# Performance work log

Measured on AMD Instinct MI355X. Metric: run time of the kernel, lower is better.

The kernel has to match this reference:

```python
import jax, jax.numpy as jnp
import numpy as np

B, T, C = 4, 2048, 1024
H = 16
DH = C // H
DFF = 4 * C


def _layernorm(x, g, b, eps=1e-5):
    mu = jnp.mean(x, axis=-1, keepdims=True)
    var = jnp.var(x, axis=-1, keepdims=True)
    return (x - mu) * jax.lax.rsqrt(var + eps) * g + b


def setup_inputs() -> dict:
    key = jax.random.key(0)
    ks = jax.random.split(key, 12)
    s = 0.02
    return {
        "x": jax.random.normal(ks[0], (B, T, C), jnp.float32),
        "Wq": jax.random.normal(ks[1], (H, C, DH), jnp.float32) * s,
        "bq": jnp.zeros((H, DH), jnp.float32),
        "Wk": jax.random.normal(ks[2], (H, C, DH), jnp.float32) * s,
        "bk": jnp.zeros((H, DH), jnp.float32),
        "Wv": jax.random.normal(ks[3], (H, C, DH), jnp.float32) * s,
        "bv": jnp.zeros((H, DH), jnp.float32),
        "Wo": jax.random.normal(ks[4], (C, C), jnp.float32) * s,
        "bo": jnp.zeros((C,), jnp.float32),
        "ln1_g": jnp.ones((C,), jnp.float32),
        "ln1_b": jnp.zeros((C,), jnp.float32),
        "ln2_g": jnp.ones((C,), jnp.float32),
        "ln2_b": jnp.zeros((C,), jnp.float32),
        "W1": jax.random.normal(ks[5], (C, DFF), jnp.float32) * s,
        "b1": jnp.zeros((DFF,), jnp.float32),
        "W2": jax.random.normal(ks[6], (DFF, C), jnp.float32) * s,
        "b2": jnp.zeros((C,), jnp.float32),
    }


def reference(x, Wq, bq, Wk, bk, Wv, bv, Wo, bo, ln1_g, ln1_b, ln2_g, ln2_b, W1, b1, W2, b2):
    # pre-norm for attention
    xn = _layernorm(x, ln1_g, ln1_b)
    # per-head projections, batched: [B,H,T,DH]
    q = jnp.einsum("btc,hcd->bhtd", xn, Wq) + bq[None, :, None, :]
    k = jnp.einsum("btc,hcd->bhtd", xn, Wk) + bk[None, :, None, :]
    v = jnp.einsum("btc,hcd->bhtd", xn, Wv) + bv[None, :, None, :]
    # FAITHFUL to source: scores / scale with scale = DH**-0.5, i.e. * sqrt(DH)
    scores = jnp.einsum("bhtd,bhsd->bhts", q, k) * jnp.sqrt(jnp.float32(DH))
    attn = jax.nn.softmax(scores, axis=-1)
    o = jnp.einsum("bhts,bhsd->bhtd", attn, v)  # [B,H,T,DH]
    # concat heads along last dim (head order matches ModuleList concat)
    o = jnp.transpose(o, (0, 2, 1, 3)).reshape(B, T, C)
    attn_out = o @ Wo + bo  # dropout is identity at eval
    x = x + attn_out
    xn2 = _layernorm(x, ln2_g, ln2_b)
    ffn = jax.nn.relu(xn2 @ W1 + b1) @ W2 + b2
    return x + ffn
```

## Files before the change

kernel.cpp:

```cpp
#include <hip/hip_runtime.h>
#include <hip/hip_bf16.h>
#include <stdint.h>

typedef unsigned short ushort_t;
typedef short short8 __attribute__((ext_vector_type(8)));
typedef unsigned short ushortx8 __attribute__((ext_vector_type(8)));
typedef float floatx4 __attribute__((ext_vector_type(4)));

__device__ __forceinline__ float b2f(ushort_t u) {
    return __uint_as_float(((unsigned int)u) << 16);
}
__device__ __forceinline__ ushort_t f2bf(float f) {
    unsigned int u = __float_as_uint(f);
    unsigned int r = u + 0x7FFFu + ((u >> 16) & 1u);
    return (ushort_t)(r >> 16);
}
__device__ __forceinline__ unsigned int cvtpk(float lo, float hi) {
    unsigned int r;
    asm("v_cvt_pk_bf16_f32 %0, %1, %2" : "=v"(r) : "v"(lo), "v"(hi));
    return r;
}
__device__ __forceinline__ void gll16(const void* g, void* l) {
    __builtin_amdgcn_global_load_lds((const __attribute__((address_space(1))) unsigned int*)g,
                                     (__attribute__((address_space(3))) unsigned int*)l,
                                     16, 0, 0);
}

__global__ void transpose_kernel(const float* __restrict__ in, ushort_t* __restrict__ out,
                                 int K, int N) {
    __shared__ float tile[32][33];
    in += (long)blockIdx.z * K * N;
    out += (long)blockIdx.z * K * N;
    int k0 = blockIdx.x * 32, n0 = blockIdx.y * 32;
    int x = threadIdx.x, y = threadIdx.y;
#pragma unroll
    for (int i = 0; i < 4; i++)
        tile[y + 8 * i][x] = in[(long)(k0 + y + 8 * i) * N + n0 + x];
    __syncthreads();
#pragma unroll
    for (int i = 0; i < 4; i++)
        out[(long)(n0 + y + 8 * i) * K + k0 + x] = f2bf(tile[x][y + 8 * i]);
}

__global__ void concat_bias_kernel(const float* __restrict__ bq, const float* __restrict__ bk,
                                   const float* __restrict__ bv, float* __restrict__ dst) {
    int i = blockIdx.x * 256 + threadIdx.x;
    dst[i] = i < 1024 ? bq[i] : (i < 2048 ? bk[i - 1024] : bv[i - 2048]);
}

__global__ __launch_bounds__(256) void ln_kernel(const float* __restrict__ in,
                                                 ushort_t* __restrict__ out,
                                                 const float* __restrict__ g,
                                                 const float* __restrict__ b) {
    long row = blockIdx.x;
    int tid = threadIdx.x;
    float4 v4 = *((const float4*)(in + row * 1024) + tid);
    float v[4] = {v4.x, v4.y, v4.z, v4.w};
    float s1 = v[0] + v[1] + v[2] + v[3];
    float s2 = v[0] * v[0] + v[1] * v[1] + v[2] * v[2] + v[3] * v[3];
#pragma unroll
    for (int m = 32; m >= 1; m >>= 1) {
        s1 += __shfl_xor(s1, m);
        s2 += __shfl_xor(s2, m);
    }
    __shared__ float r1[4], r2[4];
    int w = tid >> 6;
    if ((tid & 63) == 0) { r1[w] = s1; r2[w] = s2; }
    __syncthreads();
    s1 = r1[0] + r1[1] + r1[2] + r1[3];
    s2 = r2[0] + r2[1] + r2[2] + r2[3];
    float mu = s1 * (1.0f / 1024.0f);
    float var = s2 * (1.0f / 1024.0f) - mu * mu;
    float inv = rsqrtf(var + 1e-5f);
    float y[4];
#pragma unroll
    for (int i = 0; i < 4; i++)
        y[i] = (v[i] - mu) * inv * g[tid * 4 + i] + b[tid * 4 + i];
    unsigned int lo = (unsigned int)f2bf(y[0]) | ((unsigned int)f2bf(y[1]) << 16);
    unsigned int hi = (unsigned int)f2bf(y[2]) | ((unsigned int)f2bf(y[3]) << 16);
    *(uint2*)(out + row * 1024 + tid * 4) = make_uint2(lo, hi);
}

template <typename OutT, int RELU, int MODE>
__device__ __forceinline__ void gemm128(
    const ushort_t* __restrict__ A, int lda,
    const ushort_t* __restrict__ Bt, int ldb, int K,
    OutT* __restrict__ C, long cBatch, int ldc,
    const float* __restrict__ bias, const float* __restrict__ resid,
    ushort_t* As, ushort_t* Bs) {
    int m0 = blockIdx.x * 128, n0 = blockIdx.y * 128;
    int tid = threadIdx.x, lane = tid & 63, w = tid >> 6;
    int ln = lane & 15, quad = lane >> 4;
    int wr = w >> 1, wc = w & 1;
    int lr = lane >> 2, lc = (lane & 3) * 8;

    auto stage = [&](int k0, int buf) {
#pragma unroll
        for (int i = 0; i < 4; i++) {
            int id = w * 4 + i;
            int blk = id & 7;
            int row = blk * 16 + lr;
            if (id < 8)
                gll16(A + (long)(m0 + row) * lda + k0 + lc, As + buf * 4096 + blk * 512);
            else
                gll16(Bt + (long)(n0 + row) * ldb + k0 + lc, Bs + buf * 4096 + blk * 512);
        }
    };

    floatx4 acc[4][4];
#pragma unroll
    for (int a = 0; a < 4; a++)
#pragma unroll
        for (int bb = 0; bb < 4; bb++) acc[a][bb] = floatx4{0, 0, 0, 0};

    stage(0, 0);
    int cur = 0;
    for (int k0 = 0; k0 < K; k0 += 32, cur ^= 1) {
        __syncthreads();
        if (k0 + 32 < K) stage(k0 + 32, cur ^ 1);
        const ushort_t* Ab = As + cur * 4096;
        const ushort_t* Bb = Bs + cur * 4096;
        short8 af[4], bf[4];
#pragma unroll
        for (int j = 0; j < 4; j++) {
            af[j] = *(const short8*)(Ab + (wr * 64 + j * 16 + ln) * 32 + quad * 8);
            bf[j] = *(const short8*)(Bb + (wc * 64 + j * 16 + ln) * 32 + quad * 8);
        }
#pragma unroll
        for (int a = 0; a < 4; a++)
#pragma unroll
            for (int bb = 0; bb < 4; bb++)
                acc[a][bb] = __builtin_amdgcn_mfma_f32_16x16x32_bf16(af[a], bf[bb], acc[a][bb], 0, 0, 0);
    }
#pragma unroll
    for (int bb = 0; bb < 4; bb++) {
        int gn = n0 + wc * 64 + bb * 16 + ln;
        float bv = bias ? bias[gn] : 0.0f;
#pragma unroll
        for (int a = 0; a < 4; a++) {
#pragma unroll
            for (int r = 0; r < 4; r++) {
                int gm = m0 + wr * 64 + a * 16 + quad * 4 + r;
                float val = acc[a][bb][r] + bv;
                if (RELU) val = fmaxf(val, 0.0f);
                if constexpr (MODE == 2) {
                    int gnl = gn & 1023;
                    long off;
                    if (gn < 2048)
                        off = (long)(gn >> 10) * 8388608 + (long)(gm >> 11) * 2097152 +
                              (long)(gm & 2047) * 1024 + gnl;
                    else
                        off = 16777216L +
                              ((((long)(gm >> 11)) * 16 + (gnl >> 6)) * 64 + (gnl & 63)) * 2048 +
                              (gm & 2047);
                    C[off] = (OutT)f2bf(val);
                } else {
                    long off = (long)(gm >> 11) * cBatch + (long)(gm & 2047) * ldc + gn;
                    if (resid) val += resid[off];
                    if constexpr (sizeof(OutT) == 2)
                        C[off] = (OutT)f2bf(val);
                    else
                        C[off] = (OutT)val;
                }
            }
        }
    }
}

__global__ __launch_bounds__(256) void gemm128_qkv_kernel(
    const ushort_t* __restrict__ A, const ushort_t* __restrict__ Bt,
    ushort_t* __restrict__ C, const float* __restrict__ bias) {
    __shared__ ushort_t As[2 * 128 * 32];
    __shared__ ushort_t Bs[2 * 128 * 32];
    gemm128<ushort_t, 0, 2>(A, 1024, Bt, 1024, 1024, C, 0, 0, bias, nullptr, As, Bs);
}

__global__ __launch_bounds__(256) void gemm128_bf16_relu_kernel(
    const ushort_t* __restrict__ A, int lda, const ushort_t* __restrict__ Bt, int ldb, int K,
    ushort_t* __restrict__ C, long cBatch, int ldc, const float* __restrict__ bias) {
    __shared__ ushort_t As[2 * 128 * 32];
    __shared__ ushort_t Bs[2 * 128 * 32];
    gemm128<ushort_t, 1, 0>(A, lda, Bt, ldb, K, C, cBatch, ldc, bias, nullptr, As, Bs);
}

__global__ __launch_bounds__(256) void gemm128_f32_kernel(
    const ushort_t* __restrict__ A, int lda, const ushort_t* __restrict__ Bt, int ldb, int K,
    float* __restrict__ C, long cBatch, int ldc,
    const float* __restrict__ bias, const float* __restrict__ resid) {
    __shared__ ushort_t As[2 * 128 * 32];
    __shared__ ushort_t Bs[2 * 128 * 32];
    gemm128<float, 0, 0>(A, lda, Bt, ldb, K, C, cBatch, ldc, bias, resid, As, Bs);
}

__global__ __launch_bounds__(512, 4) void attn_kernel(
    const ushort_t* __restrict__ q, const ushort_t* __restrict__ k,
    const ushort_t* __restrict__ vt, ushort_t* __restrict__ o) {
    __shared__ ushort_t Klds[2 * 4096];
    __shared__ ushort_t Vlds[2 * 4096];
    int flat = blockIdx.x;
    int bh = (flat & 7) * 8 + (flat >> 6);
    int xt = (flat >> 3) & 7;
    int b = bh >> 4, h = bh & 15;
    int t0 = xt * 256;
    int tid = threadIdx.x, lane = tid & 63, w = tid >> 6;
    int ln = lane & 15, quad = lane >> 4;
    int lr = lane >> 2, lq = lane & 3;
    int bsrc = (lane & 48) + ((lane >> 4) << 2);
    int rsw = (ln >> 1) & 3;
    int ssw = (lr >> 1) & 3;

    const ushort_t* qbase = q + ((long)b * 2048 + t0 + w * 32) * 1024 + h * 64;
    short8 qf[2][2];
#pragma unroll
    for (int sub = 0; sub < 2; sub++)
#pragma unroll
        for (int s = 0; s < 2; s++) {
            ushortx8 t = *(const ushortx8*)(qbase + (long)(sub * 16 + ln) * 1024 + s * 32 + quad * 8);
#pragma unroll
            for (int j = 0; j < 8; j++) qf[sub][s][j] = (short)f2bf(b2f(t[j]) * 8.0f);
        }

    floatx4 O[2][4];
    float m_i[2] = {-1e30f, -1e30f}, l_i[2] = {0.0f, 0.0f};
#pragma unroll
    for (int sub = 0; sub < 2; sub++)
#pragma unroll
        for (int i = 0; i < 4; i++) O[sub][i] = floatx4{0, 0, 0, 0};

    long krow0 = (long)b * 2048 * 1024 + h * 64;
    const ushort_t* vbase = vt + (long)bh * 64 * 2048;

    auto stage = [&](int kv0, int buf) {
#pragma unroll
        for (int i = 0; i < 2; i++) {
            int id = w * 2 + i;
            int s = (id >> 2) & 1, qt = id & 3;
            int cs = ((lq ^ ssw) << 3);
            if (id < 8) {
                int prow = ((qt >> 1) << 5) + ((lr >> 2) << 3) + ((qt & 1) << 2) + (lr & 3);
                gll16(k + krow0 + (long)(kv0 + prow) * 1024 + s * 32 + cs,
                      Klds + buf * 4096 + s * 2048 + qt * 512);
            } else {
                int row = qt * 16 + lr;
                gll16(vbase + (long)row * 2048 + kv0 + s * 32 + cs,
                      Vlds + buf * 4096 + s * 2048 + qt * 512);
            }
        }
    };

    stage(0, 0);
    int cur = 0;
    for (int t32 = 0; t32 < 32; t32++, cur ^= 1) {
        __syncthreads();
        if (t32 < 31) stage((t32 + 1) * 64, cur ^ 1);
        const ushort_t* Kb = Klds + cur * 4096;
        const ushort_t* Vb = Vlds + cur * 4096;

        floatx4 Z[2][4];
#pragma unroll
        for (int sub = 0; sub < 2; sub++)
#pragma unroll
            for (int nc = 0; nc < 4; nc++) Z[sub][nc] = floatx4{0, 0, 0, 0};
#pragma unroll
        for (int s = 0; s < 2; s++)
#pragma unroll
            for (int nc = 0; nc < 4; nc++) {
                short8 kf = *(const short8*)(Kb + s * 2048 + (nc * 16 + ln) * 32 + ((quad ^ rsw) << 3));
                Z[0][nc] = __builtin_amdgcn_mfma_f32_16x16x32_bf16(kf, qf[0][s], Z[0][nc], 0, 0, 0);
                Z[1][nc] = __builtin_amdgcn_mfma_f32_16x16x32_bf16(kf, qf[1][s], Z[1][nc], 0, 0, 0);
            }

        float alpha[2];
        short8 pf[2][2];
#pragma unroll
        for (int sub = 0; sub < 2; sub++) {
            float mx = -1e30f;
#pragma unroll
            for (int nc = 0; nc < 4; nc++)
#pragma unroll
                for (int r = 0; r < 4; r++) mx = fmaxf(mx, Z[sub][nc][r]);
            mx = fmaxf(mx, __shfl_xor(mx, 16));
            mx = fmaxf(mx, __shfl_xor(mx, 32));
            float nm = fmaxf(m_i[sub], mx);
            alpha[sub] = __expf(m_i[sub] - nm);
            m_i[sub] = nm;
            float rs = 0.0f;
#pragma unroll
            for (int s = 0; s < 2; s++) {
                float a0 = __expf(Z[sub][2 * s][0] - nm), a1 = __expf(Z[sub][2 * s][1] - nm);
                float a2 = __expf(Z[sub][2 * s][2] - nm), a3 = __expf(Z[sub][2 * s][3] - nm);
                float b0 = __expf(Z[sub][2 * s + 1][0] - nm), b1 = __expf(Z[sub][2 * s + 1][1] - nm);
                float b2 = __expf(Z[sub][2 * s + 1][2] - nm), b3 = __expf(Z[sub][2 * s + 1][3] - nm);
                rs += ((a0 + a1) + (a2 + a3)) + ((b0 + b1) + (b2 + b3));
                union { unsigned int u[4]; short8 v; } pu;
                pu.u[0] = cvtpk(a0, a1);
                pu.u[1] = cvtpk(a2, a3);
                pu.u[2] = cvtpk(b0, b1);
                pu.u[3] = cvtpk(b2, b3);
                pf[sub][s] = pu.v;
            }
            rs += __shfl_xor(rs, 16);
            rs += __shfl_xor(rs, 32);
            l_i[sub] = l_i[sub] * alpha[sub] + rs;
        }
#pragma unroll
        for (int sub = 0; sub < 2; sub++)
#pragma unroll
            for (int r = 0; r < 4; r++) {
                float ar = __shfl(alpha[sub], bsrc + r);
#pragma unroll
                for (int dc = 0; dc < 4; dc++) O[sub][dc][r] *= ar;
            }
#pragma unroll
        for (int s = 0; s < 2; s++)
#pragma unroll
            for (int dc = 0; dc < 4; dc++) {
                short8 vf = *(const short8*)(Vb + s * 2048 + (dc * 16 + ln) * 32 + ((quad ^ rsw) << 3));
                O[0][dc] = __builtin_amdgcn_mfma_f32_16x16x32_bf16(pf[0][s], vf, O[0][dc], 0, 0, 0);
                O[1][dc] = __builtin_amdgcn_mfma_f32_16x16x32_bf16(pf[1][s], vf, O[1][dc], 0, 0, 0);
            }
    }
#pragma unroll
    for (int sub = 0; sub < 2; sub++)
#pragma unroll
        for (int r = 0; r < 4; r++) {
            float inv = 1.0f / __shfl(l_i[sub], bsrc + r);
            int t = t0 + w * 32 + sub * 16 + quad * 4 + r;
            ushort_t* orow = o + ((long)b * 2048 + t) * 1024 + h * 64;
#pragma unroll
            for (int dc = 0; dc < 4; dc++) orow[dc * 16 + ln] = f2bf(O[sub][dc][r] * inv);
        }
}

extern "C" void kernel_launch(void* const* d_in, const int* in_sizes, int n_in,
                              void* d_out, int out_size, void* d_ws, size_t ws_size,
                              hipStream_t stream) {
    const float* x   = (const float*)d_in[0];
    const float* Wq  = (const float*)d_in[1];
    const float* bq  = (const float*)d_in[2];
    const float* Wk  = (const float*)d_in[3];
    const float* bk  = (const float*)d_in[4];
    const float* Wv  = (const float*)d_in[5];
    const float* bv  = (const float*)d_in[6];
    const float* Wo  = (const float*)d_in[7];
    const float* bo  = (const float*)d_in[8];
    const float* g1  = (const float*)d_in[9];
    const float* be1 = (const float*)d_in[10];
    const float* g2  = (const float*)d_in[11];
    const float* be2 = (const float*)d_in[12];
    const float* W1  = (const float*)d_in[13];
    const float* b1  = (const float*)d_in[14];
    const float* W2  = (const float*)d_in[15];
    const float* b2  = (const float*)d_in[16];
    float* out = (float*)d_out;

    const long MB = 1 << 20;
    char* w = (char*)d_ws;
    ushort_t* xn  = (ushort_t*)(w);
    float*    x2  = (float*)(w + 16 * MB);
    ushort_t* qb  = (ushort_t*)(w + 48 * MB);
    ushort_t* kb  = (ushort_t*)(w + 64 * MB);
    ushort_t* vtb = (ushort_t*)(w + 80 * MB);
    ushort_t* xn2 = qb;
    ushort_t* h1  = (ushort_t*)(w + 64 * MB);
    ushort_t* WqT = (ushort_t*)(w + 96 * MB);
    ushort_t* WkT = (ushort_t*)(w + 98 * MB);
    ushort_t* WvT = (ushort_t*)(w + 100 * MB);
    ushort_t* WoT = (ushort_t*)(w + 102 * MB);
    ushort_t* W1T = (ushort_t*)(w + 104 * MB);
    ushort_t* W2T = (ushort_t*)(w + 112 * MB);
    float* biasCat = x2;

    dim3 tb(32, 8);
    transpose_kernel<<<dim3(32, 2, 16), tb, 0, stream>>>(Wq, WqT, 1024, 64);
    transpose_kernel<<<dim3(32, 2, 16), tb, 0, stream>>>(Wk, WkT, 1024, 64);
    transpose_kernel<<<dim3(32, 2, 16), tb, 0, stream>>>(Wv, WvT, 1024, 64);
    transpose_kernel<<<dim3(32, 32, 1), tb, 0, stream>>>(Wo, WoT, 1024, 1024);
    transpose_kernel<<<dim3(32, 128, 1), tb, 0, stream>>>(W1, W1T, 1024, 4096);
    transpose_kernel<<<dim3(128, 32, 1), tb, 0, stream>>>(W2, W2T, 4096, 1024);
    concat_bias_kernel<<<12, 256, 0, stream>>>(bq, bk, bv, biasCat);

    ln_kernel<<<8192, 256, 0, stream>>>(x, xn, g1, be1);
    gemm128_qkv_kernel<<<dim3(64, 24), 256, 0, stream>>>(xn, WqT, qb, biasCat);
    attn_kernel<<<512, 512, 0, stream>>>(qb, kb, vtb, xn );
    gemm128_f32_kernel<<<dim3(64, 8), 256, 0, stream>>>(xn, 1024, WoT, 1024, 1024,
                                                        x2, 2048L * 1024, 1024, bo, x);
    ln_kernel<<<8192, 256, 0, stream>>>((const float*)x2, xn2, g2, be2);
    gemm128_bf16_relu_kernel<<<dim3(64, 16), 256, 0, stream>>>(
        xn2, 1024, W1T, 1024, 1024, h1, 2048L * 2048, 2048, b1);
    gemm128_f32_kernel<<<dim3(64, 8), 256, 0, stream>>>(
        h1, 2048, W2T, 4096, 2048, out, 2048L * 1024, 1024, b2, x2);
    gemm128_bf16_relu_kernel<<<dim3(64, 16), 256, 0, stream>>>(
        xn2, 1024, W1T + 2048L * 1024, 1024, 1024, h1, 2048L * 2048, 2048, b1 + 2048);
    gemm128_f32_kernel<<<dim3(64, 8), 256, 0, stream>>>(
        h1, 2048, W2T + 2048, 4096, 2048, out, 2048L * 1024, 1024, nullptr, out);
}
```

Before: 594.2 us.

## Add 256x256 GEMM with 4-stage LDS pipeline for QKV and FFN-up

Introduces a new gemm256 kernel with 512 threads and 256x256 output tiles. It uses a four-buffer global_load_lds pipeline with manual vmcnt waits, barriers and setprio around the MFMA phases, plus an XCD-aware block remap. The QKV projection and both W1 ReLU GEMMs now use it, while the Wo and W2 GEMMs stay on the 128-tile kernel. Larger tiles raise data reuse per load and the deeper pipeline hides memory latency, at the cost of more registers and LDS. The fixed grids of 384 and 256 blocks can underfill the CUs.

```diff
diff --git a/kernel.cpp b/kernel.cpp
--- a/kernel.cpp
+++ b/kernel.cpp
@@ -6,6 +6,9 @@
 typedef short short8 __attribute__((ext_vector_type(8)));
 typedef unsigned short ushortx8 __attribute__((ext_vector_type(8)));
 typedef float floatx4 __attribute__((ext_vector_type(4)));
+
+template <int N> struct IC { static constexpr int value = N; };
+template <bool B> struct BC { static constexpr bool value = B; };
 
 __device__ __forceinline__ float b2f(ushort_t u) {
     return __uint_as_float(((unsigned int)u) << 16);
@@ -143,9 +146,138 @@
                 int gm = m0 + wr * 64 + a * 16 + quad * 4 + r;
                 float val = acc[a][bb][r] + bv;
                 if (RELU) val = fmaxf(val, 0.0f);
+                long off = (long)(gm >> 11) * cBatch + (long)(gm & 2047) * ldc + gn;
+                if (resid) val += resid[off];
+                if constexpr (sizeof(OutT) == 2)
+                    C[off] = (OutT)f2bf(val);
+                else
+                    C[off] = (OutT)val;
+            }
+        }
+    }
+}
+
+__global__ __launch_bounds__(256) void gemm128_f32_kernel(
+    const ushort_t* __restrict__ A, int lda, const ushort_t* __restrict__ Bt, int ldb, int K,
+    float* __restrict__ C, long cBatch, int ldc,
+    const float* __restrict__ bias, const float* __restrict__ resid) {
+    __shared__ ushort_t As[2 * 128 * 32];
+    __shared__ ushort_t Bs[2 * 128 * 32];
+    gemm128<float, 0, 0>(A, lda, Bt, ldb, K, C, cBatch, ldc, bias, resid, As, Bs);
+}
+
+template <int RELU, int MODE>
+__device__ __forceinline__ void gemm256(
+    const ushort_t* __restrict__ A, int lda,
+    const ushort_t* __restrict__ Bt, int ldb, int K, int ntn,
+    ushort_t* __restrict__ C, long cBatch, int ldc,
+    const float* __restrict__ bias, ushort_t* lds) {
+    int nwg = gridDim.x;
+    int wg = ((int)blockIdx.x & 7) * (nwg >> 3) + ((int)blockIdx.x >> 3);
+    int m0 = (wg / ntn) * 256, n0 = (wg % ntn) * 256;
+    int tid = threadIdx.x, lane = tid & 63, w = tid >> 6;
+    int ln = lane & 15, quad = lane >> 4;
+    int wm = w >> 2, wn = w & 3;
+    int lr = lane >> 2, lq = lane & 3;
+    int ssw = (lr >> 1) & 3, rsw = (ln >> 1) & 3;
+
+    const ushort_t* pa[2];
+    const ushort_t* pb[2];
+#pragma unroll
+    for (int i = 0; i < 2; i++) {
+        int id = w * 2 + i;
+        pa[i] = A + (long)(m0 + id * 16 + lr) * lda + ((lq ^ ssw) << 3);
+        pb[i] = Bt + (long)(n0 + id * 16 + lr) * ldb + ((lq ^ ssw) << 3);
+    }
+    auto stageA = [&](int t) {
+        ushort_t* d = lds + (t & 3) * 16384;
+#pragma unroll
+        for (int i = 0; i < 2; i++) gll16(pa[i] + t * 32, d + (w * 2 + i) * 512);
+    };
+    auto stageB = [&](int t) {
+        ushort_t* d = lds + (t & 3) * 16384 + 8192;
+#pragma unroll
+        for (int i = 0; i < 2; i++) gll16(pb[i] + t * 32, d + (w * 2 + i) * 512);
+    };
+
+    floatx4 acc[8][4];
+#pragma unroll
+    for (int a = 0; a < 8; a++)
+#pragma unroll
+        for (int bb = 0; bb < 4; bb++) acc[a][bb] = floatx4{0, 0, 0, 0};
+
+    stageA(0); stageB(0); stageA(1); stageB(1); stageA(2); stageB(2);
+    asm volatile("s_waitcnt vmcnt(8)" ::: "memory");
+    __builtin_amdgcn_s_barrier();
+    __builtin_amdgcn_sched_barrier(0);
+
+    int NT = K >> 5;
+    auto iter = [&](int t, auto vmc, auto stc) {
+        constexpr int VM = decltype(vmc)::value;
+        constexpr bool ST = decltype(stc)::value;
+        const ushort_t* Ab = lds + (t & 3) * 16384;
+        const ushort_t* Bb = Ab + 8192;
+        short8 af[4], bf[4];
+#pragma unroll
+        for (int j = 0; j < 4; j++)
+            bf[j] = *(const short8*)(Bb + (wn * 64 + j * 16 + ln) * 32 + ((quad ^ rsw) << 3));
+#pragma unroll
+        for (int j = 0; j < 4; j++)
+            af[j] = *(const short8*)(Ab + (wm * 128 + j * 16 + ln) * 32 + ((quad ^ rsw) << 3));
+        if constexpr (ST) stageA(t + 3);
+        __builtin_amdgcn_s_barrier();
+        __builtin_amdgcn_sched_barrier(0);
+        __builtin_amdgcn_s_setprio(1);
+#pragma unroll
+        for (int a = 0; a < 4; a++)
+#pragma unroll
+            for (int bb = 0; bb < 4; bb++)
+                acc[a][bb] = __builtin_amdgcn_mfma_f32_16x16x32_bf16(af[a], bf[bb], acc[a][bb], 0, 0, 0);
+        __builtin_amdgcn_s_setprio(0);
+        __builtin_amdgcn_s_barrier();
+        __builtin_amdgcn_sched_barrier(0);
+#pragma unroll
+        for (int j = 0; j < 4; j++)
+            af[j] = *(const short8*)(Ab + (wm * 128 + 64 + j * 16 + ln) * 32 + ((quad ^ rsw) << 3));
+        if constexpr (ST) stageB(t + 3);
+        __builtin_amdgcn_s_barrier();
+        __builtin_amdgcn_sched_barrier(0);
+        __builtin_amdgcn_s_setprio(1);
+#pragma unroll
+        for (int a = 0; a < 4; a++)
+#pragma unroll
+            for (int bb = 0; bb < 4; bb++)
+                acc[a + 4][bb] = __builtin_amdgcn_mfma_f32_16x16x32_bf16(af[a], bf[bb], acc[a + 4][bb], 0, 0, 0);
+        __builtin_amdgcn_s_setprio(0);
+        if constexpr (VM == 8)
+            asm volatile("s_waitcnt vmcnt(8)" ::: "memory");
+        else if constexpr (VM == 4)
+            asm volatile("s_waitcnt vmcnt(4)" ::: "memory");
+        else
+            asm volatile("s_waitcnt vmcnt(0)" ::: "memory");
+        __builtin_amdgcn_s_barrier();
+        __builtin_amdgcn_sched_barrier(0);
+    };
+
+    for (int t = 0; t < NT - 3; ++t) iter(t, IC<8>{}, BC<true>{});
+    iter(NT - 3, IC<4>{}, BC<false>{});
+    iter(NT - 2, IC<0>{}, BC<false>{});
+    iter(NT - 1, IC<0>{}, BC<false>{});
+
+#pragma unroll
+    for (int bb = 0; bb < 4; bb++) {
+        int gn = n0 + wn * 64 + bb * 16 + ln;
+        float bv = bias[gn];
+#pragma unroll
+        for (int a = 0; a < 8; a++) {
+#pragma unroll
+            for (int r = 0; r < 4; r++) {
+                int gm = m0 + wm * 128 + a * 16 + quad * 4 + r;
+                float val = acc[a][bb][r] + bv;
+                if (RELU) val = fmaxf(val, 0.0f);
+                long off;
                 if constexpr (MODE == 2) {
                     int gnl = gn & 1023;
-                    long off;
                     if (gn < 2048)
                         off = (long)(gn >> 10) * 8388608 + (long)(gm >> 11) * 2097152 +
                               (long)(gm & 2047) * 1024 + gnl;
@@ -153,43 +285,27 @@
                         off = 16777216L +
                               ((((long)(gm >> 11)) * 16 + (gnl >> 6)) * 64 + (gnl & 63)) * 2048 +
                               (gm & 2047);
-                    C[off] = (OutT)f2bf(val);
                 } else {
-                    long off = (long)(gm >> 11) * cBatch + (long)(gm & 2047) * ldc + gn;
-                    if (resid) val += resid[off];
-                    if constexpr (sizeof(OutT) == 2)
-                        C[off] = (OutT)f2bf(val);
-                    else
-                        C[off] = (OutT)val;
+                    off = (long)(gm >> 11) * cBatch + (long)(gm & 2047) * ldc + gn;
                 }
+                C[off] = f2bf(val);
             }
         }
     }
 }
 
-__global__ __launch_bounds__(256) void gemm128_qkv_kernel(
+__global__ __launch_bounds__(512, 2) void gemm256_qkv_kernel(
     const ushort_t* __restrict__ A, const ushort_t* __restrict__ Bt,
     ushort_t* __restrict__ C, const float* __restrict__ bias) {
-    __shared__ ushort_t As[2 * 128 * 32];
-    __shared__ ushort_t Bs[2 * 128 * 32];
-    gemm128<ushort_t, 0, 2>(A, 1024, Bt, 1024, 1024, C, 0, 0, bias, nullptr, As, Bs);
-}
-
-__global__ __launch_bounds__(256) void gemm128_bf16_relu_kernel(
-    const ushort_t* __restrict__ A, int lda, const ushort_t* __restrict__ Bt, int ldb, int K,
-    ushort_t* __restrict__ C, long cBatch, int ldc, const float* __restrict__ bias) {
-    __shared__ ushort_t As[2 * 128 * 32];
-    __shared__ ushort_t Bs[2 * 128 * 32];
-    gemm128<ushort_t, 1, 0>(A, lda, Bt, ldb, K, C, cBatch, ldc, bias, nullptr, As, Bs);
-}
-
-__global__ __launch_bounds__(256) void gemm128_f32_kernel(
-    const ushort_t* __restrict__ A, int lda, const ushort_t* __restrict__ Bt, int ldb, int K,
-    float* __restrict__ C, long cBatch, int ldc,
-    const float* __restrict__ bias, const float* __restrict__ resid) {
-    __shared__ ushort_t As[2 * 128 * 32];
-    __shared__ ushort_t Bs[2 * 128 * 32];
-    gemm128<float, 0, 0>(A, lda, Bt, ldb, K, C, cBatch, ldc, bias, resid, As, Bs);
+    __shared__ ushort_t lds[4 * 16384];
+    gemm256<0, 2>(A, 1024, Bt, 1024, 1024, 12, C, 0, 0, bias, lds);
+}
+
+__global__ __launch_bounds__(512, 2) void gemm256_relu_kernel(
+    const ushort_t* __restrict__ A, const ushort_t* __restrict__ Bt,
+    ushort_t* __restrict__ C, const float* __restrict__ bias) {
+    __shared__ ushort_t lds[4 * 16384];
+    gemm256<1, 0>(A, 1024, Bt, 1024, 1024, 8, C, 2048L * 2048, 2048, bias, lds);
 }
 
 __global__ __launch_bounds__(512, 4) void attn_kernel(
@@ -381,17 +497,15 @@
     concat_bias_kernel<<<12, 256, 0, stream>>>(bq, bk, bv, biasCat);
 
     ln_kernel<<<8192, 256, 0, stream>>>(x, xn, g1, be1);
-    gemm128_qkv_kernel<<<dim3(64, 24), 256, 0, stream>>>(xn, WqT, qb, biasCat);
+    gemm256_qkv_kernel<<<384, 512, 0, stream>>>(xn, WqT, qb, biasCat);
     attn_kernel<<<512, 512, 0, stream>>>(qb, kb, vtb, xn );
     gemm128_f32_kernel<<<dim3(64, 8), 256, 0, stream>>>(xn, 1024, WoT, 1024, 1024,
                                                         x2, 2048L * 1024, 1024, bo, x);
     ln_kernel<<<8192, 256, 0, stream>>>((const float*)x2, xn2, g2, be2);
-    gemm128_bf16_relu_kernel<<<dim3(64, 16), 256, 0, stream>>>(
-        xn2, 1024, W1T, 1024, 1024, h1, 2048L * 2048, 2048, b1);
+    gemm256_relu_kernel<<<256, 512, 0, stream>>>(xn2, W1T, h1, b1);
     gemm128_f32_kernel<<<dim3(64, 8), 256, 0, stream>>>(
         h1, 2048, W2T, 4096, 2048, out, 2048L * 1024, 1024, b2, x2);
-    gemm128_bf16_relu_kernel<<<dim3(64, 16), 256, 0, stream>>>(
-        xn2, 1024, W1T + 2048L * 1024, 1024, 1024, h1, 2048L * 2048, 2048, b1 + 2048);
+    gemm256_relu_kernel<<<256, 512, 0, stream>>>(xn2, W1T + 2048L * 1024, h1, b1 + 2048);
     gemm128_f32_kernel<<<dim3(64, 8), 256, 0, stream>>>(
         h1, 2048, W2T + 2048, 4096, 2048, out, 2048L * 1024, 1024, nullptr, out);
 }
```

After: 592.6 us. About the same (-0.3%).

## Triple-buffer GEMM LDS with swizzled layout, raw barriers and XCD-aware tile mapping

Applied to the files above, without the earlier changes.

Changes the shared GEMM from double to triple buffering, keeping two global-to-LDS stages in flight with explicit vmcnt waits and raw s_barrier instead of __syncthreads. LDS columns are XOR-swizzled on write and read to avoid bank conflicts, and source pointers are precomputed once. Launches become 1D with an XCD-aware remap of block index to tile, so neighbouring tiles share L2 on the same chiplet. LDS use per block grows to 48KB, and the hand-placed waitcnt/barrier sequence must stay correct.

```diff
diff --git a/kernel.cpp b/kernel.cpp
--- a/kernel.cpp
+++ b/kernel.cpp
@@ -6,6 +6,8 @@
 typedef short short8 __attribute__((ext_vector_type(8)));
 typedef unsigned short ushortx8 __attribute__((ext_vector_type(8)));
 typedef float floatx4 __attribute__((ext_vector_type(4)));
+
+#define SBAR() asm volatile("s_barrier" ::: "memory")
 
 __device__ __forceinline__ float b2f(ushort_t u) {
     return __uint_as_float(((unsigned int)u) << 16);
@@ -87,24 +89,28 @@
     const ushort_t* __restrict__ Bt, int ldb, int K,
     OutT* __restrict__ C, long cBatch, int ldc,
     const float* __restrict__ bias, const float* __restrict__ resid,
-    ushort_t* As, ushort_t* Bs) {
-    int m0 = blockIdx.x * 128, n0 = blockIdx.y * 128;
+    ushort_t* As, ushort_t* Bs, int mT, int nT) {
+    int m0 = mT * 128, n0 = nT * 128;
     int tid = threadIdx.x, lane = tid & 63, w = tid >> 6;
     int ln = lane & 15, quad = lane >> 4;
     int wr = w >> 1, wc = w & 1;
-    int lr = lane >> 2, lc = (lane & 3) * 8;
-
-    auto stage = [&](int k0, int buf) {
-#pragma unroll
-        for (int i = 0; i < 4; i++) {
-            int id = w * 4 + i;
-            int blk = id & 7;
-            int row = blk * 16 + lr;
-            if (id < 8)
-                gll16(A + (long)(m0 + row) * lda + k0 + lc, As + buf * 4096 + blk * 512);
-            else
-                gll16(Bt + (long)(n0 + row) * ldb + k0 + lc, Bs + buf * 4096 + blk * 512);
-        }
+    int lr = lane >> 2, lq = lane & 3;
+    int ssw = (lr >> 1) & 3, rsw = (ln >> 1) & 3;
+
+    const ushort_t* src[4];
+    ushort_t* dstb[4];
+#pragma unroll
+    for (int i = 0; i < 4; i++) {
+        int id = w * 4 + i;
+        int blk = id & 7;
+        int row = blk * 16 + lr;
+        src[i] = (id < 8 ? A + (long)(m0 + row) * lda
+                         : Bt + (long)(n0 + row) * ldb) + ((lq ^ ssw) << 3);
+        dstb[i] = (id < 8 ? As : Bs) + blk * 512;
+    }
+    auto stage = [&](int t, int buf) {
+#pragma unroll
+        for (int i = 0; i < 4; i++) gll16(src[i] + t * 32, dstb[i] + buf * 4096);
     };
 
     floatx4 acc[4][4];
@@ -113,25 +119,40 @@
 #pragma unroll
         for (int bb = 0; bb < 4; bb++) acc[a][bb] = floatx4{0, 0, 0, 0};
 
+    int NT = K >> 5;
     stage(0, 0);
-    int cur = 0;
-    for (int k0 = 0; k0 < K; k0 += 32, cur ^= 1) {
-        __syncthreads();
-        if (k0 + 32 < K) stage(k0 + 32, cur ^ 1);
+    stage(1, 1);
+    asm volatile("s_waitcnt vmcnt(4)" ::: "memory");
+    SBAR();
+
+    int cur = 0, bst = 2;
+    auto body = [&](int t, int doStage, int vm) {
+        if (doStage) stage(t + 2, bst);
         const ushort_t* Ab = As + cur * 4096;
         const ushort_t* Bb = Bs + cur * 4096;
         short8 af[4], bf[4];
 #pragma unroll
         for (int j = 0; j < 4; j++) {
-            af[j] = *(const short8*)(Ab + (wr * 64 + j * 16 + ln) * 32 + quad * 8);
-            bf[j] = *(const short8*)(Bb + (wc * 64 + j * 16 + ln) * 32 + quad * 8);
+            af[j] = *(const short8*)(Ab + (wr * 64 + j * 16 + ln) * 32 + ((quad ^ rsw) << 3));
+            bf[j] = *(const short8*)(Bb + (wc * 64 + j * 16 + ln) * 32 + ((quad ^ rsw) << 3));
         }
 #pragma unroll
         for (int a = 0; a < 4; a++)
 #pragma unroll
             for (int bb = 0; bb < 4; bb++)
                 acc[a][bb] = __builtin_amdgcn_mfma_f32_16x16x32_bf16(af[a], bf[bb], acc[a][bb], 0, 0, 0);
-    }
+        if (vm == 4)
+            asm volatile("s_waitcnt vmcnt(4)" ::: "memory");
+        else if (vm == 0)
+            asm volatile("s_waitcnt vmcnt(0)" ::: "memory");
+        SBAR();
+        cur = cur == 2 ? 0 : cur + 1;
+        bst = bst == 2 ? 0 : bst + 1;
+    };
+    for (int t = 0; t < NT - 2; ++t) body(t, 1, 4);
+    body(NT - 2, 0, 0);
+    body(NT - 1, 0, -1);
+
 #pragma unroll
     for (int bb = 0; bb < 4; bb++) {
         int gn = n0 + wc * 64 + bb * 16 + ln;
@@ -167,29 +188,39 @@
     }
 }
 
-__global__ __launch_bounds__(256) void gemm128_qkv_kernel(
+__device__ __forceinline__ int xcd_swz(int flat, int nwg) {
+    return (flat & 7) * (nwg >> 3) + (flat >> 3);
+}
+
+__global__ __launch_bounds__(256, 3) void gemm128_qkv_kernel(
     const ushort_t* __restrict__ A, const ushort_t* __restrict__ Bt,
     ushort_t* __restrict__ C, const float* __restrict__ bias) {
-    __shared__ ushort_t As[2 * 128 * 32];
-    __shared__ ushort_t Bs[2 * 128 * 32];
-    gemm128<ushort_t, 0, 2>(A, 1024, Bt, 1024, 1024, C, 0, 0, bias, nullptr, As, Bs);
-}
-
-__global__ __launch_bounds__(256) void gemm128_bf16_relu_kernel(
+    __shared__ ushort_t As[3 * 4096];
+    __shared__ ushort_t Bs[3 * 4096];
+    int wg = xcd_swz(blockIdx.x, gridDim.x);
+    gemm128<ushort_t, 0, 2>(A, 1024, Bt, 1024, 1024, C, 0, 0, bias, nullptr,
+                            As, Bs, wg & 63, wg >> 6);
+}
+
+__global__ __launch_bounds__(256, 3) void gemm128_relu_kernel(
     const ushort_t* __restrict__ A, int lda, const ushort_t* __restrict__ Bt, int ldb, int K,
     ushort_t* __restrict__ C, long cBatch, int ldc, const float* __restrict__ bias) {
-    __shared__ ushort_t As[2 * 128 * 32];
-    __shared__ ushort_t Bs[2 * 128 * 32];
-    gemm128<ushort_t, 1, 0>(A, lda, Bt, ldb, K, C, cBatch, ldc, bias, nullptr, As, Bs);
-}
-
-__global__ __launch_bounds__(256) void gemm128_f32_kernel(
+    __shared__ ushort_t As[3 * 4096];
+    __shared__ ushort_t Bs[3 * 4096];
+    int wg = xcd_swz(blockIdx.x, gridDim.x);
+    gemm128<ushort_t, 1, 0>(A, lda, Bt, ldb, K, C, cBatch, ldc, bias, nullptr,
+                            As, Bs, wg & 63, wg >> 6);
+}
+
+__global__ __launch_bounds__(256, 3) void gemm128_f32_kernel(
     const ushort_t* __restrict__ A, int lda, const ushort_t* __restrict__ Bt, int ldb, int K,
     float* __restrict__ C, long cBatch, int ldc,
     const float* __restrict__ bias, const float* __restrict__ resid) {
-    __shared__ ushort_t As[2 * 128 * 32];
-    __shared__ ushort_t Bs[2 * 128 * 32];
-    gemm128<float, 0, 0>(A, lda, Bt, ldb, K, C, cBatch, ldc, bias, resid, As, Bs);
+    __shared__ ushort_t As[3 * 4096];
+    __shared__ ushort_t Bs[3 * 4096];
+    int wg = xcd_swz(blockIdx.x, gridDim.x);
+    gemm128<float, 0, 0>(A, lda, Bt, ldb, K, C, cBatch, ldc, bias, resid,
+                         As, Bs, wg & 63, wg >> 6);
 }
 
 __global__ __launch_bounds__(512, 4) void attn_kernel(
@@ -381,17 +412,17 @@
     concat_bias_kernel<<<12, 256, 0, stream>>>(bq, bk, bv, biasCat);
 
     ln_kernel<<<8192, 256, 0, stream>>>(x, xn, g1, be1);
-    gemm128_qkv_kernel<<<dim3(64, 24), 256, 0, stream>>>(xn, WqT, qb, biasCat);
+    gemm128_qkv_kernel<<<1536, 256, 0, stream>>>(xn, WqT, qb, biasCat);
     attn_kernel<<<512, 512, 0, stream>>>(qb, kb, vtb, xn );
-    gemm128_f32_kernel<<<dim3(64, 8), 256, 0, stream>>>(xn, 1024, WoT, 1024, 1024,
-                                                        x2, 2048L * 1024, 1024, bo, x);
+    gemm128_f32_kernel<<<512, 256, 0, stream>>>(xn, 1024, WoT, 1024, 1024,
+                                                x2, 2048L * 1024, 1024, bo, x);
     ln_kernel<<<8192, 256, 0, stream>>>((const float*)x2, xn2, g2, be2);
-    gemm128_bf16_relu_kernel<<<dim3(64, 16), 256, 0, stream>>>(
+    gemm128_relu_kernel<<<1024, 256, 0, stream>>>(
         xn2, 1024, W1T, 1024, 1024, h1, 2048L * 2048, 2048, b1);
-    gemm128_f32_kernel<<<dim3(64, 8), 256, 0, stream>>>(
+    gemm128_f32_kernel<<<512, 256, 0, stream>>>(
         h1, 2048, W2T, 4096, 2048, out, 2048L * 1024, 1024, b2, x2);
-    gemm128_bf16_relu_kernel<<<dim3(64, 16), 256, 0, stream>>>(
+    gemm128_relu_kernel<<<1024, 256, 0, stream>>>(
         xn2, 1024, W1T + 2048L * 1024, 1024, 1024, h1, 2048L * 2048, 2048, b1 + 2048);
-    gemm128_f32_kernel<<<dim3(64, 8), 256, 0, stream>>>(
+    gemm128_f32_kernel<<<512, 256, 0, stream>>>(
         h1, 2048, W2T + 2048, 4096, 2048, out, 2048L * 1024, 1024, nullptr, out);
 }
```

Measured after the change: 633.8 us. +6.7%, slower.
